# Performance work log

Measured on AMD Instinct MI355X. Metric: run time of the kernel, lower is better.

The kernel has to match this reference:

```python
import jax, jax.numpy as jnp
import numpy as np

EPS = 1e-5
DIM, QK, PDIM, SR = 256, 64, 128, 2
B, H, W = 16, 64, 64
SCALE = QK ** (-0.5)


def _conv(x, w, stride, pad, groups=1):
    return jax.lax.conv_general_dilated(
        x, w, (stride, stride), [(pad, pad), (pad, pad)], feature_group_count=groups)


def _bn(x, g, b, m, v):
    # inference-mode BatchNorm2d with running stats
    s = (g / jnp.sqrt(v + EPS))[None, :, None, None]
    return (x - m[None, :, None, None]) * s + b[None, :, None, None]


def _gn1(x, g, b):
    # GroupNorm(1, C): normalize over (C,H,W) per sample
    mu = x.mean(axis=(1, 2, 3), keepdims=True)
    var = x.var(axis=(1, 2, 3), keepdims=True)
    xh = (x - mu) / jnp.sqrt(var + EPS)
    return xh * g[None, :, None, None] + b[None, :, None, None]


def setup_inputs() -> dict:
    key = jax.random.key(0)
    ks = jax.random.split(key, 6)
    inp = {
        'x': jax.random.normal(ks[0], (B, DIM, H, W), jnp.float32),
        'gn_g': jnp.ones((DIM,), jnp.float32),
        'gn_b': jnp.zeros((DIM,), jnp.float32),
        'w_in': jax.random.normal(ks[1], (2 * QK + DIM, DIM, 3, 3), jnp.float32) * 0.05,
        'bn_in_g': jnp.ones((2 * QK + DIM,), jnp.float32),
        'bn_in_b': jnp.zeros((2 * QK + DIM,), jnp.float32),
        'bn_in_m': jnp.zeros((2 * QK + DIM,), jnp.float32),
        'bn_in_v': jnp.ones((2 * QK + DIM,), jnp.float32),
        'w_k': jax.random.normal(ks[2], (QK, 1, SR, SR), jnp.float32) * 0.05,
        'bn_k_g': jnp.ones((QK,), jnp.float32),
        'bn_k_b': jnp.zeros((QK,), jnp.float32),
        'bn_k_m': jnp.zeros((QK,), jnp.float32),
        'bn_k_v': jnp.ones((QK,), jnp.float32),
        'w_v': jax.random.normal(ks[3], (PDIM, 1, SR, SR), jnp.float32) * 0.05,
        'bn_v_g': jnp.ones((PDIM,), jnp.float32),
        'bn_v_b': jnp.zeros((PDIM,), jnp.float32),
        'bn_v_m': jnp.zeros((PDIM,), jnp.float32),
        'bn_v_v': jnp.ones((PDIM,), jnp.float32),
        'w_out': jax.random.normal(ks[4], (DIM, DIM, 1, 1), jnp.float32) * 0.05,
        'bn_out_g': jnp.ones((DIM,), jnp.float32),
        'bn_out_b': jnp.zeros((DIM,), jnp.float32),
        'bn_out_m': jnp.zeros((DIM,), jnp.float32),
        'bn_out_v': jnp.ones((DIM,), jnp.float32),
    }
    return inp


def reference(x, gn_g, gn_b, w_in, bn_in_g, bn_in_b, bn_in_m, bn_in_v,
              w_k, bn_k_g, bn_k_b, bn_k_m, bn_k_v,
              w_v, bn_v_g, bn_v_b, bn_v_m, bn_v_v,
              w_out, bn_out_g, bn_out_b, bn_out_m, bn_out_v):
    x = _gn1(x, gn_g, gn_b)
    y = _bn(_conv(x, w_in, 1, 1), bn_in_g, bn_in_b, bn_in_m, bn_in_v)
    q = y[:, :QK]
    k = y[:, QK:2 * QK]
    v = y[:, 2 * QK:2 * QK + PDIM]
    u = y[:, 2 * QK + PDIM:]
    # depthwise sr-stride convs reduce k/v spatially
    k = _bn(_conv(k, w_k, SR, 0, groups=QK), bn_k_g, bn_k_b, bn_k_m, bn_k_v)
    v = _bn(_conv(v, w_v, SR, 0, groups=PDIM), bn_v_g, bn_v_b, bn_v_m, bn_v_v)
    b, _, h, w = u.shape
    qf = q.reshape(b, QK, -1)      # [B, QK, N]
    kf = k.reshape(b, QK, -1)      # [B, QK, M]
    vf = v.reshape(b, PDIM, -1)    # [B, PDIM, M]
    attn = jnp.einsum('bcn,bcm->bnm', qf, kf) * SCALE
    attn = jax.nn.softmax(attn, axis=-1)
    o = jnp.einsum('bcm,bnm->bcn', vf, attn).reshape(b, PDIM, h, w)
    cat = jnp.concatenate([o, u], axis=1)
    out = _bn(_conv(jax.nn.relu(cat), w_out, 1, 0), bn_out_g, bn_out_b, bn_out_m, bn_out_v)
    return out
```

## Files before the change

### kernel.cpp

```cpp
#include <hip/hip_runtime.h>
#include <stdint.h>

#define EPSV 1e-5f

typedef __attribute__((ext_vector_type(8))) short short8;
typedef __attribute__((ext_vector_type(4))) float f32x4;
typedef __bf16 bf16x8 __attribute__((ext_vector_type(8)));

__device__ __forceinline__ unsigned short f2bf(float f) {
  union { float f; unsigned int u; } v; v.f = f;
  unsigned int r = (v.u + 0x7FFFu + ((v.u >> 16) & 1u)) >> 16;
  return (unsigned short)r;
}
__device__ __forceinline__ float bf2f(unsigned short h) {
  union { unsigned int u; float f; } v; v.u = ((unsigned int)h) << 16;
  return v.f;
}

__device__ __forceinline__ f32x4 mfma16(bf16x8 a, bf16x8 b, f32x4 c) {
  return __builtin_amdgcn_mfma_f32_16x16x32_bf16(a, b, c, 0, 0, 0);
}

#define GLOAD16(g, l)                                                          \
  __builtin_amdgcn_global_load_lds(                                            \
      (const __attribute__((address_space(1))) void*)(g),                      \
      (__attribute__((address_space(3))) void*)(l), 16, 0, 0)

__global__ __launch_bounds__(256) void k_gn_stats(const float* __restrict__ x,
                                                  float* __restrict__ stats) {
  int b = blockIdx.x >> 6, chunk = blockIdx.x & 63;
  const float4* xp = (const float4*)(x + ((size_t)b << 20) + (size_t)chunk * 16384);
  int t = threadIdx.x;
  float s = 0.f, q = 0.f;
#pragma unroll
  for (int i = 0; i < 16; ++i) {
    float4 v = xp[i * 256 + t];
    s += v.x + v.y + v.z + v.w;
    q += v.x * v.x + v.y * v.y + v.z * v.z + v.w * v.w;
  }
#pragma unroll
  for (int m = 1; m <= 32; m <<= 1) { s += __shfl_xor(s, m); q += __shfl_xor(q, m); }
  __shared__ float ls[8];
  int w = t >> 6, l = t & 63;
  if (l == 0) { ls[w * 2] = s; ls[w * 2 + 1] = q; }
  __syncthreads();
  if (t == 0) {
    float S = ls[0] + ls[2] + ls[4] + ls[6];
    float Q = ls[1] + ls[3] + ls[5] + ls[7];
    atomicAdd(&stats[b * 2], S);
    atomicAdd(&stats[b * 2 + 1], Q);
  }
}

__global__ __launch_bounds__(256) void k_gn_norm(const float* __restrict__ x,
                                                 const float* __restrict__ stats,
                                                 const float* __restrict__ g,
                                                 const float* __restrict__ bb,
                                                 unsigned short* __restrict__ xnp) {
  __shared__ float tile[64][65];
  int pt = blockIdx.x;
  int ct = blockIdx.y;
  int b = blockIdx.z;
  int t = threadIdx.x, tr = t >> 6, tc = t & 63;
  const float* xb = x + ((size_t)b << 20) + (size_t)(ct * 64) * 4096 + pt * 64;
#pragma unroll
  for (int i = 0; i < 16; ++i) {
    int r = i * 4 + tr;
    tile[r][tc] = xb[(size_t)r * 4096 + tc];
  }
  __syncthreads();
  float mu = stats[b * 2] * (1.f / 1048576.f);
  float var = stats[b * 2 + 1] * (1.f / 1048576.f) - mu * mu;
  float istd = rsqrtf(var + EPSV);
  float gg = g[ct * 64 + tc] * istd;
  float bv = bb[ct * 64 + tc];
  unsigned short* out = xnp + (((size_t)b * 66 + (pt + 1)) * 66 + 1) * 256 + ct * 64 + tc;
#pragma unroll
  for (int i = 0; i < 16; ++i) {
    int pcol = i * 4 + tr;
    float v = (tile[tc][pcol] - mu) * gg + bv;
    out[(size_t)pcol * 256] = f2bf(v);
  }
}

__global__ __launch_bounds__(256) void k_prep_wt(const float* __restrict__ w_in,
                                                 const float* __restrict__ bg,
                                                 const float* __restrict__ bv,
                                                 unsigned short* __restrict__ wt) {
  int idx = blockIdx.x * 256 + threadIdx.x;
  if (idx >= 9 * 384 * 256) return;
  int tap = idx / 98304;
  int rem = idx - tap * 98304;
  int co = rem >> 8, ci = rem & 255;
  float s = bg[co] * rsqrtf(bv[co] + EPSV);
  wt[idx] = f2bf(w_in[(size_t)(co * 256 + ci) * 9 + tap] * s);
}

__global__ __launch_bounds__(256) void k_prep_misc(
    const float* w_out, const float* og, const float* ob, const float* om, const float* ov,
    const float* big, const float* bib, const float* bim, const float* biv,
    const float* w_k, const float* kg, const float* kb, const float* km, const float* kvv,
    const float* w_v, const float* vg, const float* vb, const float* vm, const float* vvv,
    unsigned short* wo2, float* bias_in, float* bias_out,
    float* wkf, float* bias_k, float* wvf, float* bias_v) {
  int idx = blockIdx.x * 256 + threadIdx.x;
  if (idx < 65536) {
    int co = idx >> 8;
    float s = og[co] * rsqrtf(ov[co] + EPSV);
    wo2[idx] = f2bf(w_out[idx] * s);
    return;
  }
  idx -= 65536;
  if (idx < 384) {
    float s = big[idx] * rsqrtf(biv[idx] + EPSV);
    bias_in[idx] = bib[idx] - bim[idx] * s;
    return;
  }
  idx -= 384;
  if (idx < 256) {
    float s = og[idx] * rsqrtf(ov[idx] + EPSV);
    bias_out[idx] = ob[idx] - om[idx] * s;
    return;
  }
  idx -= 256;
  if (idx < 64) {
    float s = kg[idx] * rsqrtf(kvv[idx] + EPSV);
#pragma unroll
    for (int tp = 0; tp < 4; ++tp) wkf[idx * 4 + tp] = w_k[idx * 4 + tp] * s;
    bias_k[idx] = kb[idx] - km[idx] * s;
    return;
  }
  idx -= 64;
  if (idx < 128) {
    float s = vg[idx] * rsqrtf(vvv[idx] + EPSV);
#pragma unroll
    for (int tp = 0; tp < 4; ++tp) wvf[idx * 4 + tp] = w_v[idx * 4 + tp] * s;
    bias_v[idx] = vb[idx] - vm[idx] * s;
    return;
  }
}

__global__ __launch_bounds__(256) void k_conv3(const unsigned short* __restrict__ xnp,
                                               const unsigned short* __restrict__ wt,
                                               const float* __restrict__ bias_in,
                                               unsigned short* __restrict__ y) {
  int pt = blockIdx.x, cot = blockIdx.y, b = blockIdx.z;
  int p0 = pt * 128, co0 = cot * 128;
  __shared__ alignas(16) unsigned short As[128 * 64];
  __shared__ alignas(16) unsigned short Bs[128 * 64];
  int t = threadIdx.x, w = t >> 6, l = t & 63;
  int rr = t >> 3, c8 = (t & 7) * 8;
  int lg = l >> 4, lr = l & 15;

  int baseA[4];
#pragma unroll
  for (int i = 0; i < 4; ++i) {
    int p = p0 + i * 32 + rr;
    int yy = p >> 6, xx = p & 63;
    baseA[i] = ((b * 66 + yy) * 66 + xx) * 256 + c8;
  }
  int baseB = (co0 + rr) * 256 + c8;

  f32x4 acc[4][4];
#pragma unroll
  for (int i = 0; i < 4; ++i)
#pragma unroll
    for (int j = 0; j < 4; ++j) acc[i][j] = f32x4{0.f, 0.f, 0.f, 0.f};

  int wr = (w >> 1) * 64, wc = (w & 1) * 64;

  for (int tap = 0; tap < 9; ++tap) {
    int aoff = ((tap / 3) * 66 + (tap % 3)) * 256;
#pragma unroll 1
    for (int kc = 0; kc < 4; ++kc) {
      int ci0 = kc * 64;
      __syncthreads();
#pragma unroll
      for (int i = 0; i < 4; ++i) {
        GLOAD16(xnp + baseA[i] + aoff + ci0, &As[(i * 32 + w * 8) * 64]);
        GLOAD16(wt + baseB + tap * 98304 + i * 8192 + ci0, &Bs[(i * 32 + w * 8) * 64]);
      }
      __syncthreads();
      bf16x8 af[4][2], bf[4][2];
#pragma unroll
      for (int mt = 0; mt < 4; ++mt)
#pragma unroll
        for (int k2 = 0; k2 < 2; ++k2) {
          af[mt][k2] = *(const bf16x8*)&As[(wr + mt * 16 + lr) * 64 + k2 * 32 + lg * 8];
          bf[mt][k2] = *(const bf16x8*)&Bs[(wc + mt * 16 + lr) * 64 + k2 * 32 + lg * 8];
        }
#pragma unroll
      for (int mt = 0; mt < 4; ++mt)
#pragma unroll
        for (int nt = 0; nt < 4; ++nt) {
          acc[mt][nt] = mfma16(af[mt][0], bf[nt][0], acc[mt][nt]);
          acc[mt][nt] = mfma16(af[mt][1], bf[nt][1], acc[mt][nt]);
        }
    }
  }
  float bias[4];
  int coBase = co0 + wc;
#pragma unroll
  for (int nt = 0; nt < 4; ++nt) bias[nt] = bias_in[coBase + nt * 16 + lr];
#pragma unroll
  for (int mt = 0; mt < 4; ++mt) {
    int p = p0 + wr + mt * 16 + lg * 4;
#pragma unroll
    for (int r = 0; r < 4; ++r) {
      size_t rowoff = ((size_t)(b * 4096 + p + r)) * 384;
#pragma unroll
      for (int nt = 0; nt < 4; ++nt) {
        int co = coBase + nt * 16 + lr;
        float v = acc[mt][nt][r] + bias[nt];
        if (co >= 256) v = fmaxf(v, 0.f);
        y[rowoff + co] = f2bf(v);
      }
    }
  }
}

__global__ __launch_bounds__(256) void k_kv(const unsigned short* __restrict__ y,
                                            const float* __restrict__ wkf, const float* __restrict__ bias_k,
                                            const float* __restrict__ wvf, const float* __restrict__ bias_v,
                                            unsigned short* __restrict__ kk, unsigned short* __restrict__ vv) {
  constexpr int LDW = 200;
  __shared__ unsigned short ty[128 * LDW];
  __shared__ unsigned short vt[128 * 33];
  int b = blockIdx.x >> 5, my = blockIdx.x & 31;
  int t = threadIdx.x;
  const unsigned short* ybase = y + ((size_t)(b * 4096 + my * 128)) * 384 + 64;
#pragma unroll
  for (int j = 0; j < 12; ++j) {
    int idx = j * 256 + t;
    int row = idx / 24, c8 = idx - row * 24;
    bf16x8 v = *(const bf16x8*)&ybase[(size_t)row * 384 + c8 * 8];
    *(bf16x8*)&ty[row * LDW + c8 * 8] = v;
  }
  __syncthreads();

  {
    int c = t & 63, wq = t >> 6;
    float wk0 = wkf[c * 4 + 0], wk1 = wkf[c * 4 + 1];
    float wk2 = wkf[c * 4 + 2], wk3 = wkf[c * 4 + 3];
    float bk = bias_k[c];
#pragma unroll
    for (int pass = 0; pass < 8; ++pass) {
      int mx = pass * 4 + wq;
      int r0 = 2 * mx, r1 = 2 * mx + 1;
      float a = bk;
      a += bf2f(ty[r0 * LDW + c]) * wk0;
      a += bf2f(ty[(r0 + 1) * LDW + c]) * wk1;
      a += bf2f(ty[(64 + r0) * LDW + c]) * wk2;
      a += bf2f(ty[(64 + r1) * LDW + c]) * wk3;
      kk[((size_t)(b * 1024 + my * 32 + mx)) * 64 + c] = f2bf(a);
    }
  }

  {
    int cv = t & 127, mxh = t >> 7;
    float wv0 = wvf[cv * 4 + 0], wv1 = wvf[cv * 4 + 1];
    float wv2 = wvf[cv * 4 + 2], wv3 = wvf[cv * 4 + 3];
    float bv = bias_v[cv];
    int col = 64 + cv;
#pragma unroll
    for (int pass = 0; pass < 16; ++pass) {
      int mx = pass * 2 + mxh;
      int r0 = 2 * mx, r1 = 2 * mx + 1;
      float a = bv;
      a += bf2f(ty[r0 * LDW + col]) * wv0;
      a += bf2f(ty[r1 * LDW + col]) * wv1;
      a += bf2f(ty[(64 + r0) * LDW + col]) * wv2;
      a += bf2f(ty[(64 + r1) * LDW + col]) * wv3;
      vt[cv * 33 + mx] = f2bf(a);
    }
  }
  __syncthreads();
  {
    int mx = t & 31, cvq = t >> 5;
#pragma unroll
    for (int i = 0; i < 16; ++i) {
      int cv = i * 8 + cvq;
      vv[((size_t)(b * 128 + cv)) * 1024 + my * 32 + mx] = vt[cv * 33 + mx];
    }
  }
}

__global__ __launch_bounds__(256) void k_attn(unsigned short* __restrict__ y,
                                              const unsigned short* __restrict__ kk,
                                              const unsigned short* __restrict__ vvb) {
  int blk = blockIdx.x;
  int b = blk >> 5, ntile = blk & 31;
  int t = threadIdx.x, w = t >> 6, l = t & 63;
  int nq0 = ntile * 128 + w * 32;
  int lg = l >> 4, lr = l & 15;
  __shared__ alignas(16) unsigned short P[4][2][16][64];
  const float SC = 0.125f * 1.44269504f;

  union { short8 s; bf16x8 b; } uo;
#pragma unroll
  for (int i = 0; i < 8; ++i) uo.s[i] = (short)0x3F80;
  bf16x8 ones = uo.b;

  bf16x8 qf[2][2];
#pragma unroll
  for (int qt = 0; qt < 2; ++qt)
#pragma unroll
    for (int c = 0; c < 2; ++c)
      qf[qt][c] = *(const bf16x8*)&y[((size_t)(b * 4096 + nq0 + qt * 16 + lr)) * 384 + c * 32 + lg * 8];

  f32x4 oa[2][8];
#pragma unroll
  for (int qt = 0; qt < 2; ++qt)
#pragma unroll
    for (int tt = 0; tt < 8; ++tt) oa[qt][tt] = f32x4{0.f, 0.f, 0.f, 0.f};
  float mi[2][4], li[2][4];
#pragma unroll
  for (int qt = 0; qt < 2; ++qt)
#pragma unroll
    for (int r = 0; r < 4; ++r) { mi[qt][r] = -1e30f; li[qt][r] = 0.f; }

  for (int m0 = 0; m0 < 1024; m0 += 64) {
    bf16x8 kf[4][2];
#pragma unroll
    for (int mt = 0; mt < 4; ++mt)
#pragma unroll
      for (int c = 0; c < 2; ++c)
        kf[mt][c] = *(const bf16x8*)&kk[((size_t)(b * 1024 + m0 + mt * 16 + lr)) * 64 + c * 32 + lg * 8];

#pragma unroll
    for (int qt = 0; qt < 2; ++qt) {
      f32x4 s[4];
#pragma unroll
      for (int mt = 0; mt < 4; ++mt) {
        f32x4 z = f32x4{0.f, 0.f, 0.f, 0.f};
        z = mfma16(qf[qt][0], kf[mt][0], z);
        z = mfma16(qf[qt][1], kf[mt][1], z);
        s[mt] = z;
      }
      float rm[4];
#pragma unroll
      for (int r = 0; r < 4; ++r) {
        s[0][r] *= SC; s[1][r] *= SC; s[2][r] *= SC; s[3][r] *= SC;
        rm[r] = fmaxf(fmaxf(s[0][r], s[1][r]), fmaxf(s[2][r], s[3][r]));
      }
#pragma unroll
      for (int msk = 1; msk <= 8; msk <<= 1)
#pragma unroll
        for (int r = 0; r < 4; ++r) rm[r] = fmaxf(rm[r], __shfl_xor(rm[r], msk));
      bool grow = (rm[0] > mi[qt][0]) | (rm[1] > mi[qt][1]) |
                  (rm[2] > mi[qt][2]) | (rm[3] > mi[qt][3]);
      if (__any(grow)) {
#pragma unroll
        for (int r = 0; r < 4; ++r) {
          float nm = fmaxf(mi[qt][r], rm[r]);
          float corr = exp2f(mi[qt][r] - nm);
          mi[qt][r] = nm;
          li[qt][r] *= corr;
#pragma unroll
          for (int tt = 0; tt < 8; ++tt) oa[qt][tt][r] *= corr;
        }
      }
#pragma unroll
      for (int mt = 0; mt < 4; ++mt)
#pragma unroll
        for (int r = 0; r < 4; ++r) {
          float e = exp2f(s[mt][r] - mi[qt][r]);
          P[w][qt][lg * 4 + r][mt * 16 + lr] = f2bf(e);
        }
    }
    __builtin_amdgcn_wave_barrier();
    bf16x8 pf[2][2];
#pragma unroll
    for (int qt = 0; qt < 2; ++qt)
#pragma unroll
      for (int mc = 0; mc < 2; ++mc)
        pf[qt][mc] = *(const bf16x8*)&P[w][qt][lr][mc * 32 + lg * 8];
#pragma unroll
    for (int qt = 0; qt < 2; ++qt) {
      f32x4 zz = f32x4{0.f, 0.f, 0.f, 0.f};
      zz = mfma16(pf[qt][0], ones, zz);
      zz = mfma16(pf[qt][1], ones, zz);
#pragma unroll
      for (int r = 0; r < 4; ++r) li[qt][r] += zz[r];
    }
#pragma unroll
    for (int tt = 0; tt < 8; ++tt) {
      bf16x8 vf0 = *(const bf16x8*)&vvb[((size_t)(b * 128 + tt * 16 + lr)) * 1024 + m0 + lg * 8];
      bf16x8 vf1 = *(const bf16x8*)&vvb[((size_t)(b * 128 + tt * 16 + lr)) * 1024 + m0 + 32 + lg * 8];
#pragma unroll
      for (int qt = 0; qt < 2; ++qt) {
        oa[qt][tt] = mfma16(pf[qt][0], vf0, oa[qt][tt]);
        oa[qt][tt] = mfma16(pf[qt][1], vf1, oa[qt][tt]);
      }
    }
  }
#pragma unroll
  for (int qt = 0; qt < 2; ++qt)
#pragma unroll
    for (int r = 0; r < 4; ++r) {
      float inv = 1.f / li[qt][r];
      int p = nq0 + qt * 16 + lg * 4 + r;
#pragma unroll
      for (int tt = 0; tt < 8; ++tt) {
        float v = oa[qt][tt][r] * inv;
        v = fmaxf(v, 0.f);
        y[((size_t)(b * 4096 + p)) * 384 + 128 + tt * 16 + lr] = f2bf(v);
      }
    }
}

__global__ __launch_bounds__(256) void k_conv1(const unsigned short* __restrict__ y,
                                               const unsigned short* __restrict__ wo2,
                                               const float* __restrict__ bias_out,
                                               float* __restrict__ out) {
  int ptile = blockIdx.x, cot = blockIdx.y, b = blockIdx.z;
  int p0 = ptile * 128, co0 = cot * 128;
  __shared__ alignas(16) unsigned short As[128 * 64];
  __shared__ alignas(16) unsigned short Bs[128 * 64];
  int t = threadIdx.x, w = t >> 6, l = t & 63;
  int rr = t >> 3, c8 = (t & 7) * 8;
  int lg = l >> 4, lr = l & 15;
  int baseA = (co0 + rr) * 256 + c8;
  size_t baseB = ((size_t)(b * 4096 + p0 + rr)) * 384 + 128 + c8;
  f32x4 acc[4][4];
#pragma unroll
  for (int i = 0; i < 4; ++i)
#pragma unroll
    for (int j = 0; j < 4; ++j) acc[i][j] = f32x4{0.f, 0.f, 0.f, 0.f};
  int wr = (w >> 1) * 64, wc = (w & 1) * 64;
#pragma unroll 1
  for (int kc = 0; kc < 4; ++kc) {
    int ci0 = kc * 64;
    __syncthreads();
#pragma unroll
    for (int i = 0; i < 4; ++i) {
      GLOAD16(wo2 + baseA + i * 8192 + ci0, &As[(i * 32 + w * 8) * 64]);
      GLOAD16(y + baseB + (size_t)i * 32 * 384 + ci0, &Bs[(i * 32 + w * 8) * 64]);
    }
    __syncthreads();
    bf16x8 af[4][2], bf[4][2];
#pragma unroll
    for (int mt = 0; mt < 4; ++mt)
#pragma unroll
      for (int k2 = 0; k2 < 2; ++k2) {
        af[mt][k2] = *(const bf16x8*)&As[(wr + mt * 16 + lr) * 64 + k2 * 32 + lg * 8];
        bf[mt][k2] = *(const bf16x8*)&Bs[(wc + mt * 16 + lr) * 64 + k2 * 32 + lg * 8];
      }
#pragma unroll
    for (int mt = 0; mt < 4; ++mt)
#pragma unroll
      for (int nt = 0; nt < 4; ++nt) {
        acc[mt][nt] = mfma16(af[mt][0], bf[nt][0], acc[mt][nt]);
        acc[mt][nt] = mfma16(af[mt][1], bf[nt][1], acc[mt][nt]);
      }
  }
#pragma unroll
  for (int mt = 0; mt < 4; ++mt)
#pragma unroll
    for (int r = 0; r < 4; ++r) {
      int co = co0 + wr + mt * 16 + lg * 4 + r;
      float bv = bias_out[co];
      size_t obase = ((size_t)(b * 256 + co)) << 12;
#pragma unroll
      for (int nt = 0; nt < 4; ++nt) {
        int p = p0 + wc + nt * 16 + lr;
        out[obase + p] = acc[mt][nt][r] + bv;
      }
    }
}

static constexpr size_t pad256(size_t x) { return (x + 255) & ~(size_t)255; }

extern "C" void kernel_launch(void* const* d_in, const int* in_sizes, int n_in,
                              void* d_out, int out_size, void* d_ws, size_t ws_size,
                              hipStream_t stream) {
  const float* x      = (const float*)d_in[0];
  const float* gn_g   = (const float*)d_in[1];
  const float* gn_b   = (const float*)d_in[2];
  const float* w_in   = (const float*)d_in[3];
  const float* bin_g  = (const float*)d_in[4];
  const float* bin_b  = (const float*)d_in[5];
  const float* bin_m  = (const float*)d_in[6];
  const float* bin_v  = (const float*)d_in[7];
  const float* w_k    = (const float*)d_in[8];
  const float* bk_g   = (const float*)d_in[9];
  const float* bk_b   = (const float*)d_in[10];
  const float* bk_m   = (const float*)d_in[11];
  const float* bk_v   = (const float*)d_in[12];
  const float* w_v    = (const float*)d_in[13];
  const float* bv_g   = (const float*)d_in[14];
  const float* bv_b   = (const float*)d_in[15];
  const float* bv_m   = (const float*)d_in[16];
  const float* bv_v   = (const float*)d_in[17];
  const float* w_out  = (const float*)d_in[18];
  const float* bo_g   = (const float*)d_in[19];
  const float* bo_b   = (const float*)d_in[20];
  const float* bo_m   = (const float*)d_in[21];
  const float* bo_v   = (const float*)d_in[22];
  float* out = (float*)d_out;

  char* ws = (char*)d_ws;
  size_t off = 0;
  float*          stats   = (float*)(ws + off);          off += pad256(128);
  unsigned short* wt      = (unsigned short*)(ws + off); off += pad256((size_t)9 * 384 * 256 * 2);
  float*          bias_in = (float*)(ws + off);          off += pad256(384 * 4);
  unsigned short* wo2     = (unsigned short*)(ws + off); off += pad256(256 * 256 * 2);
  float*          bias_out= (float*)(ws + off);          off += pad256(256 * 4);
  float*          wkf     = (float*)(ws + off);          off += pad256(64 * 4 * 4);
  float*          bias_k  = (float*)(ws + off);          off += pad256(64 * 4);
  float*          wvf     = (float*)(ws + off);          off += pad256(128 * 4 * 4);
  float*          bias_v  = (float*)(ws + off);          off += pad256(128 * 4);
  unsigned short* xnp     = (unsigned short*)(ws + off); off += pad256((size_t)16 * 66 * 66 * 256 * 2);
  unsigned short* y       = (unsigned short*)(ws + off); off += pad256((size_t)16 * 4096 * 384 * 2);
  unsigned short* kk      = (unsigned short*)(ws + off); off += pad256((size_t)16 * 1024 * 64 * 2);
  unsigned short* vv      = (unsigned short*)(ws + off); off += pad256((size_t)16 * 128 * 1024 * 2);
  (void)ws_size; (void)out_size; (void)n_in; (void)in_sizes;

  hipMemsetAsync(stats, 0, 256, stream);
  hipMemsetAsync(xnp, 0, (size_t)16 * 66 * 66 * 256 * 2, stream);

  k_gn_stats<<<1024, 256, 0, stream>>>(x, stats);
  k_prep_wt<<<3456, 256, 0, stream>>>(w_in, bin_g, bin_v, wt);
  k_prep_misc<<<260, 256, 0, stream>>>(w_out, bo_g, bo_b, bo_m, bo_v,
                                       bin_g, bin_b, bin_m, bin_v,
                                       w_k, bk_g, bk_b, bk_m, bk_v,
                                       w_v, bv_g, bv_b, bv_m, bv_v,
                                       wo2, bias_in, bias_out, wkf, bias_k, wvf, bias_v);
  k_gn_norm<<<dim3(64, 4, 16), 256, 0, stream>>>(x, stats, gn_g, gn_b, xnp);
  k_conv3<<<dim3(32, 3, 16), 256, 0, stream>>>(xnp, wt, bias_in, y);
  k_kv<<<512, 256, 0, stream>>>(y, wkf, bias_k, wvf, bias_v, kk, vv);
  k_attn<<<512, 256, 0, stream>>>(y, kk, vv);
  k_conv1<<<dim3(32, 2, 16), 256, 0, stream>>>(y, wo2, bias_out, out);
}
```

Measured before the change: 515.2 us.

## Restructure attention kernel with LDS-staged K tiles and transposed P reads

```diff
diff --git a/kernel.cpp b/kernel.cpp
--- a/kernel.cpp
+++ b/kernel.cpp
@@ -19,6 +19,12 @@
 
 __device__ __forceinline__ f32x4 mfma16(bf16x8 a, bf16x8 b, f32x4 c) {
   return __builtin_amdgcn_mfma_f32_16x16x32_bf16(a, b, c, 0, 0, 0);
+}
+
+__device__ __forceinline__ unsigned cvt_pk_bf16(float lo, float hi) {
+  unsigned r;
+  asm("v_cvt_pk_bf16_f32 %0, %1, %2" : "=v"(r) : "v"(lo), "v"(hi));
+  return r;
 }
 
 #define GLOAD16(g, l)                                                          \
@@ -285,15 +291,16 @@
   }
 }
 
-__global__ __launch_bounds__(256) void k_attn(unsigned short* __restrict__ y,
-                                              const unsigned short* __restrict__ kk,
-                                              const unsigned short* __restrict__ vvb) {
+__global__ __launch_bounds__(512, 4) void k_attn(unsigned short* __restrict__ y,
+                                                 const unsigned short* __restrict__ kk,
+                                                 const unsigned short* __restrict__ vvb) {
+  __shared__ alignas(16) unsigned short Ks[2][4096];
+  __shared__ alignas(16) unsigned short PT[8][64][16];
   int blk = blockIdx.x;
   int b = blk >> 5, ntile = blk & 31;
   int t = threadIdx.x, w = t >> 6, l = t & 63;
-  int nq0 = ntile * 128 + w * 32;
   int lg = l >> 4, lr = l & 15;
-  __shared__ alignas(16) unsigned short P[4][2][16][64];
+  int nq0 = ntile * 128 + w * 16;
   const float SC = 0.125f * 1.44269504f;
 
   union { short8 s; bf16x8 b; } uo;
@@ -301,112 +308,130 @@
   for (int i = 0; i < 8; ++i) uo.s[i] = (short)0x3F80;
   bf16x8 ones = uo.b;
 
-  bf16x8 qf[2][2];
-#pragma unroll
-  for (int qt = 0; qt < 2; ++qt)
-#pragma unroll
-    for (int c = 0; c < 2; ++c)
-      qf[qt][c] = *(const bf16x8*)&y[((size_t)(b * 4096 + nq0 + qt * 16 + lr)) * 384 + c * 32 + lg * 8];
-
-  f32x4 oa[2][8];
-#pragma unroll
-  for (int qt = 0; qt < 2; ++qt)
-#pragma unroll
-    for (int tt = 0; tt < 8; ++tt) oa[qt][tt] = f32x4{0.f, 0.f, 0.f, 0.f};
-  float mi[2][4], li[2][4];
-#pragma unroll
-  for (int qt = 0; qt < 2; ++qt)
-#pragma unroll
-    for (int r = 0; r < 4; ++r) { mi[qt][r] = -1e30f; li[qt][r] = 0.f; }
-
-  for (int m0 = 0; m0 < 1024; m0 += 64) {
-    bf16x8 kf[4][2];
+  bf16x8 qf[2];
+#pragma unroll
+  for (int c = 0; c < 2; ++c)
+    qf[c] = *(const bf16x8*)&y[((size_t)(b * 4096 + nq0 + lr)) * 384 + c * 32 + lg * 8];
+
+  f32x4 oa[8];
+#pragma unroll
+  for (int tt = 0; tt < 8; ++tt) oa[tt] = f32x4{0.f, 0.f, 0.f, 0.f};
+  float mi[4], li[4];
+#pragma unroll
+  for (int r = 0; r < 4; ++r) { mi[r] = -1e30f; li[r] = 0.f; }
+
+  int srow = t >> 3;
+  int skg = (t & 7) ^ (srow & 7);
+  const unsigned short* ksrc = kk + ((size_t)(b * 1024 + srow)) * 64 + skg * 8;
+  unsigned short* ldst0 = &Ks[0][w * 512];
+  unsigned short* ldst1 = &Ks[1][w * 512];
+
+  GLOAD16(ksrc, ldst0);
+  __syncthreads();
+
+  for (int it = 0; it < 16; ++it) {
+    int cur = it & 1;
+    const unsigned short* Kc = &Ks[cur][0];
+    if (it < 15) GLOAD16(ksrc + (it + 1) * 4096, cur ? ldst0 : ldst1);
+
+    f32x4 s[4];
+#pragma unroll
+    for (int mt = 0; mt < 4; ++mt) {
+      int row = mt * 16 + lr;
+      int sw = (lr & 7) << 3;
+      bf16x8 kf0 = *(const bf16x8*)&Kc[row * 64 + ((lg * 8) ^ sw)];
+      bf16x8 kf1 = *(const bf16x8*)&Kc[row * 64 + ((32 + lg * 8) ^ sw)];
+      f32x4 z = f32x4{0.f, 0.f, 0.f, 0.f};
+      z = mfma16(qf[0], kf0, z);
+      z = mfma16(qf[1], kf1, z);
+      s[mt] = z;
+    }
+
+    float rm[4];
+#pragma unroll
+    for (int r = 0; r < 4; ++r)
+      rm[r] = fmaxf(fmaxf(s[0][r], s[1][r]), fmaxf(s[2][r], s[3][r]));
+#pragma unroll
+    for (int msk = 1; msk <= 8; msk <<= 1)
+#pragma unroll
+      for (int r = 0; r < 4; ++r) rm[r] = fmaxf(rm[r], __shfl_xor(rm[r], msk));
+    bool grow = false;
+#pragma unroll
+    for (int r = 0; r < 4; ++r) grow |= (rm[r] * SC > mi[r]);
+    if (__any(grow)) {
+#pragma unroll
+      for (int r = 0; r < 4; ++r) {
+        float nm = fmaxf(mi[r], rm[r] * SC);
+        float corr = exp2f(mi[r] - nm);
+        mi[r] = nm;
+        li[r] *= corr;
+#pragma unroll
+        for (int tt = 0; tt < 8; ++tt) oa[tt][r] *= corr;
+      }
+    }
 #pragma unroll
     for (int mt = 0; mt < 4; ++mt)
 #pragma unroll
-      for (int c = 0; c < 2; ++c)
-        kf[mt][c] = *(const bf16x8*)&kk[((size_t)(b * 1024 + m0 + mt * 16 + lr)) * 64 + c * 32 + lg * 8];
-
-#pragma unroll
-    for (int qt = 0; qt < 2; ++qt) {
-      f32x4 s[4];
-#pragma unroll
-      for (int mt = 0; mt < 4; ++mt) {
-        f32x4 z = f32x4{0.f, 0.f, 0.f, 0.f};
-        z = mfma16(qf[qt][0], kf[mt][0], z);
-        z = mfma16(qf[qt][1], kf[mt][1], z);
-        s[mt] = z;
-      }
-      float rm[4];
-#pragma unroll
-      for (int r = 0; r < 4; ++r) {
-        s[0][r] *= SC; s[1][r] *= SC; s[2][r] *= SC; s[3][r] *= SC;
-        rm[r] = fmaxf(fmaxf(s[0][r], s[1][r]), fmaxf(s[2][r], s[3][r]));
-      }
-#pragma unroll
-      for (int msk = 1; msk <= 8; msk <<= 1)
-#pragma unroll
-        for (int r = 0; r < 4; ++r) rm[r] = fmaxf(rm[r], __shfl_xor(rm[r], msk));
-      bool grow = (rm[0] > mi[qt][0]) | (rm[1] > mi[qt][1]) |
-                  (rm[2] > mi[qt][2]) | (rm[3] > mi[qt][3]);
-      if (__any(grow)) {
-#pragma unroll
-        for (int r = 0; r < 4; ++r) {
-          float nm = fmaxf(mi[qt][r], rm[r]);
-          float corr = exp2f(mi[qt][r] - nm);
-          mi[qt][r] = nm;
-          li[qt][r] *= corr;
-#pragma unroll
-          for (int tt = 0; tt < 8; ++tt) oa[qt][tt][r] *= corr;
-        }
-      }
-#pragma unroll
-      for (int mt = 0; mt < 4; ++mt)
-#pragma unroll
-        for (int r = 0; r < 4; ++r) {
-          float e = exp2f(s[mt][r] - mi[qt][r]);
-          P[w][qt][lg * 4 + r][mt * 16 + lr] = f2bf(e);
-        }
-    }
-    __builtin_amdgcn_wave_barrier();
-    bf16x8 pf[2][2];
-#pragma unroll
-    for (int qt = 0; qt < 2; ++qt)
-#pragma unroll
-      for (int mc = 0; mc < 2; ++mc)
-        pf[qt][mc] = *(const bf16x8*)&P[w][qt][lr][mc * 32 + lg * 8];
-#pragma unroll
-    for (int qt = 0; qt < 2; ++qt) {
+      for (int r = 0; r < 4; ++r)
+        s[mt][r] = exp2f(fmaf(s[mt][r], SC, -mi[r]));
+
+#pragma unroll
+    for (int mt = 0; mt < 4; ++mt) {
+      unsigned p01 = cvt_pk_bf16(s[mt][0], s[mt][1]);
+      unsigned p23 = cvt_pk_bf16(s[mt][2], s[mt][3]);
+      unsigned long long pk = ((unsigned long long)p23 << 32) | p01;
+      *(unsigned long long*)&PT[w][mt * 16 + lr][lg * 4] = pk;
+    }
+    asm volatile("s_waitcnt lgkmcnt(0)" ::: "memory");
+
+    bf16x8 pf[2];
+#pragma unroll
+    for (int kc = 0; kc < 2; ++kc) {
+      unsigned base = (unsigned)(uintptr_t)&PT[w][kc * 32 + lg * 8][lr];
+      unsigned r0x, r0y, r1x, r1y;
+      uint2 t0, t1;
+      asm volatile("ds_read_b64_tr_b16 %0, %1" : "=v"(t0) : "v"(base));
+      asm volatile("ds_read_b64_tr_b16 %0, %1 offset:128" : "=v"(t1) : "v"(base));
+      union { unsigned u[4]; bf16x8 b; } cv;
+      cv.u[0] = t0.x; cv.u[1] = t0.y; cv.u[2] = t1.x; cv.u[3] = t1.y;
+      pf[kc] = cv.b;
+      (void)r0x; (void)r0y; (void)r1x; (void)r1y;
+    }
+    asm volatile("s_waitcnt lgkmcnt(0)" ::: "memory");
+    __builtin_amdgcn_sched_barrier(0);
+
+    {
       f32x4 zz = f32x4{0.f, 0.f, 0.f, 0.f};
-      zz = mfma16(pf[qt][0], ones, zz);
-      zz = mfma16(pf[qt][1], ones, zz);
-#pragma unroll
-      for (int r = 0; r < 4; ++r) li[qt][r] += zz[r];
-    }
+      zz = mfma16(pf[0], ones, zz);
+      zz = mfma16(pf[1], ones, zz);
+#pragma unroll
+      for (int r = 0; r < 4; ++r) li[r] += zz[r];
+    }
+
+    size_t vbase = ((size_t)(b * 128)) * 1024 + it * 64 + lg * 8;
 #pragma unroll
     for (int tt = 0; tt < 8; ++tt) {
-      bf16x8 vf0 = *(const bf16x8*)&vvb[((size_t)(b * 128 + tt * 16 + lr)) * 1024 + m0 + lg * 8];
-      bf16x8 vf1 = *(const bf16x8*)&vvb[((size_t)(b * 128 + tt * 16 + lr)) * 1024 + m0 + 32 + lg * 8];
-#pragma unroll
-      for (int qt = 0; qt < 2; ++qt) {
-        oa[qt][tt] = mfma16(pf[qt][0], vf0, oa[qt][tt]);
-        oa[qt][tt] = mfma16(pf[qt][1], vf1, oa[qt][tt]);
-      }
-    }
-  }
-#pragma unroll
-  for (int qt = 0; qt < 2; ++qt)
-#pragma unroll
-    for (int r = 0; r < 4; ++r) {
-      float inv = 1.f / li[qt][r];
-      int p = nq0 + qt * 16 + lg * 4 + r;
-#pragma unroll
-      for (int tt = 0; tt < 8; ++tt) {
-        float v = oa[qt][tt][r] * inv;
-        v = fmaxf(v, 0.f);
-        y[((size_t)(b * 4096 + p)) * 384 + 128 + tt * 16 + lr] = f2bf(v);
-      }
-    }
+      const unsigned short* vr = &vvb[vbase + (size_t)(tt * 16 + lr) * 1024];
+      bf16x8 vf0 = *(const bf16x8*)&vr[0];
+      bf16x8 vf1 = *(const bf16x8*)&vr[32];
+      oa[tt] = mfma16(pf[0], vf0, oa[tt]);
+      oa[tt] = mfma16(pf[1], vf1, oa[tt]);
+    }
+    __syncthreads();
+  }
+
+#pragma unroll
+  for (int r = 0; r < 4; ++r) {
+    float inv = 1.f / li[r];
+    int p = nq0 + lg * 4 + r;
+    size_t rowoff = ((size_t)(b * 4096 + p)) * 384 + 128;
+#pragma unroll
+    for (int tt = 0; tt < 8; ++tt) {
+      float v = oa[tt][r] * inv;
+      v = fmaxf(v, 0.f);
+      y[rowoff + tt * 16 + lr] = f2bf(v);
+    }
+  }
 }
 
 __global__ __launch_bounds__(256) void k_conv1(const unsigned short* __restrict__ y,
@@ -529,6 +554,6 @@
   k_gn_norm<<<dim3(64, 4, 16), 256, 0, stream>>>(x, stats, gn_g, gn_b, xnp);
   k_conv3<<<dim3(32, 3, 16), 256, 0, stream>>>(xnp, wt, bias_in, y);
   k_kv<<<512, 256, 0, stream>>>(y, wkf, bias_k, wvf, bias_v, kk, vv);
-  k_attn<<<512, 256, 0, stream>>>(y, kk, vv);
+  k_attn<<<512, 512, 0, stream>>>(y, kk, vv);
   k_conv1<<<dim3(32, 2, 16), 256, 0, stream>>>(y, wo2, bias_out, out);
 }
```

Result: faster. 469.1 us (-8.9%).
